# Performance work log

Hardware: AMD Instinct MI355X
Metric: run time of the kernel (lower is better)

Reference implementation:

```python
import jax, jax.numpy as jnp
import numpy as np

F, V, D, B = 3, 512, 8192, 64


def setup_inputs() -> dict:
    key = jax.random.key(0)
    k1, k2 = jax.random.split(key)
    # bipolar (MAP) codebooks: (f, v, d) in {-1, +1}
    codebooks = jnp.sign(jax.random.normal(k1, (F, V, D), dtype=jnp.float32))
    codebooks = jnp.where(codebooks == 0, 1.0, codebooks)
    # ground-truth factors -> inputs = bind (elementwise product) of one codevector per factor
    idx = jax.random.randint(k2, (B, F), 0, V)
    picked = codebooks[jnp.arange(F)[None, :], idx]          # (b, f, d)
    inputs = jnp.prod(picked, axis=1)                         # (b, d)
    # init estimates: bundle (superposition) of each codebook, signed, broadcast to batch
    init = jnp.sign(jnp.sum(codebooks, axis=1))               # (f, d)
    init = jnp.where(init == 0, 1.0, init)
    init_estimates = jnp.broadcast_to(init, (B, F, D)).astype(jnp.float32)
    return {"inputs": inputs, "init_estimates": init_estimates,
            "codebooks": codebooks, "iterations": 10}


def reference(inputs, init_estimates, codebooks, iterations):
    f = init_estimates.shape[-2]

    def step(est):
        # MAP inverse is identity; inv_others[:, j] = prod_{i != j} est[:, i]
        rolled = jnp.stack([jnp.roll(est, i, axis=-2) for i in range(1, f)], axis=-2)  # (b,f,f-1,d)
        inv_others = jnp.prod(rolled, axis=-2)                 # (b, f, d)  multibind
        new_est = inputs[:, None, :] * inv_others              # bind       (b, f, d)
        sim = jnp.einsum('bfd,fvd->bfv', new_est, codebooks)   # codebook similarity
        return jnp.sign(jnp.einsum('bfv,fvd->bfd', sim, codebooks))

    def cond(c):
        est, old, cnt, done = c
        return (cnt < iterations) & jnp.logical_not(done)

    def body(c):
        est, old, cnt, done = c
        new = step(est)
        done = jnp.all(new == old)
        return (new, new, cnt + 1, done)

    carry0 = (init_estimates, init_estimates, jnp.int32(0), jnp.array(False))
    est, _, cnt, _ = jax.lax.while_loop(cond, body, carry0)

    # cleanup: nearest codevector per factor (argmax dot similarity)
    sims = jnp.einsum('bfd,fvd->bfv', est, codebooks)
    outcome = jnp.argmax(sims, axis=-1)                        # (b, f) int indices
    return outcome, cnt - 1
```

## Files before the change

kernel.cpp:

```cpp
#include <hip/hip_runtime.h>

#define F 3
#define V 512
#define D 8192
#define B 64
#define ITERS 10
#define DW 256

typedef __bf16 bf16_t;
typedef __bf16 bf16x8 __attribute__((ext_vector_type(8)));
typedef float f32x4 __attribute__((ext_vector_type(4)));
typedef unsigned int u32;
typedef unsigned long long u64;


__global__ __launch_bounds__(256) void k_init_tr(const float* __restrict__ Csrc,
                                                 bf16_t* __restrict__ CbT,
                                                 u32* __restrict__ Cbits) {
  int f = blockIdx.z, vt = blockIdx.y, dt = blockIdx.x;
  __shared__ bf16_t tile[64 * 65];
  int t = threadIdx.x;
  int lane = t & 63;
  int v0 = vt * 64, d0 = dt * 64;
#pragma unroll
  for (int p = 0; p < 16; ++p) {
    int q = t + 256 * p;
    int i = q >> 6, j = q & 63;
    float x = Csrc[((long)(f * V + v0 + i)) * D + d0 + j];
    tile[i * 65 + j] = (bf16_t)x;
    u64 bal = __ballot(x < 0.f);
    if (lane == 0) {
      int v = v0 + i;
      uint2 wp;
      wp.x = (u32)(bal & 0xffffffffull);
      wp.y = (u32)(bal >> 32);
      *(uint2*)&Cbits[(((f * 64 + (dt >> 1)) * 512) + v) * 4 + (dt & 1) * 2] = wp;
    }
  }
  __syncthreads();
#pragma unroll
  for (int p = 0; p < 16; ++p) {
    int q = t + 256 * p;
    int jj = q >> 6, ii = q & 63;
    CbT[((long)f * D + d0 + jj) * V + v0 + ii] = tile[ii * 65 + jj];
  }
}

__global__ void k_init_pack(const float* __restrict__ inputs, const float* __restrict__ ie,
                            u32* __restrict__ in_bits, u32* __restrict__ es0,
                            u32* __restrict__ ez0, int* __restrict__ flags) {
  int tid = blockIdx.x * blockDim.x + threadIdx.x;
  int lane = tid & 63;
  int gw = tid >> 6;
  int NW = (gridDim.x * blockDim.x) >> 6;
  const int IN_W = B * (D / 64);
  const int EST_W = B * F * (D / 64);
  for (int c = gw; c < IN_W + EST_W; c += NW) {
    if (c < IN_W) {
      int b = c >> 7, dc = c & 127;
      float x = inputs[(long)b * D + dc * 64 + lane];
      u64 bal = __ballot(x < 0.f);
      if (lane == 0) {
        in_bits[b * DW + dc * 2] = (u32)(bal & 0xffffffffull);
        in_bits[b * DW + dc * 2 + 1] = (u32)(bal >> 32);
      }
    } else {
      int cc = c - IN_W;
      int bf = cc >> 7, dc = cc & 127;
      float x = ie[(long)bf * D + dc * 64 + lane];
      u64 bs = __ballot(x < 0.f);
      u64 bz = __ballot(x == 0.f);
      if (lane == 0) {
        es0[bf * DW + dc * 2] = (u32)(bs & 0xffffffffull);
        es0[bf * DW + dc * 2 + 1] = (u32)(bs >> 32);
        ez0[bf * DW + dc * 2] = (u32)(bz & 0xffffffffull);
        ez0[bf * DW + dc * 2 + 1] = (u32)(bz >> 32);
      }
    }
  }
  if (tid < 32) flags[tid] = 0;
}

__global__ __launch_bounds__(256) void k_sim(const u32* __restrict__ Cbits,
                                             const u32* __restrict__ in_bits,
                                             const u32* __restrict__ es0,
                                             const u32* __restrict__ ez0,
                                             const u32* __restrict__ es1,
                                             const u32* __restrict__ ez1,
                                             int* __restrict__ simBase,
                                             const int* __restrict__ anydiff,
                                             const int* __restrict__ hzp, int iter) {
  const int t = threadIdx.x, lane = t & 63;
  const int gw = blockIdx.x * 4 + (t >> 6);
  const int vg = gw & 7, bp = (gw >> 3) & 31, f = gw >> 8;
  const int b0 = bp * 2;
  const bool is_final = (iter >= ITERS);
  const u32 *es, *ez;
  int* sim;
  if (is_final) {
    int first0 = ITERS;
    for (int i = 0; i < ITERS; ++i)
      if (anydiff[i] == 0) { first0 = i; break; }
    int par = (first0 < ITERS) ? ((first0 + 1) & 1) : 0;
    es = par ? es1 : es0;
    ez = par ? ez1 : ez0;
    sim = simBase + ITERS * (F * B * V);
  } else {
    for (int i = 0; i < iter; ++i)
      if (anydiff[i] == 0) return;
    es = (iter & 1) ? es1 : es0;
    ez = (iter & 1) ? ez1 : ez0;
    sim = simBase + iter * (F * B * V);
  }
  const int hz = *hzp;

  u32 As0[4], As1[4], Az0[4], Az1[4];
  if (is_final) {
    const int i0 = (b0 * F + f) * DW, i1 = ((b0 + 1) * F + f) * DW;
#pragma unroll
    for (int r = 0; r < 4; ++r) {
      int o = r * 64 + lane;
      As0[r] = es[i0 + o];
      As1[r] = es[i1 + o];
    }
    if (hz) {
#pragma unroll
      for (int r = 0; r < 4; ++r) {
        int o = r * 64 + lane;
        Az0[r] = ~ez[i0 + o];
        Az1[r] = ~ez[i1 + o];
      }
    }
  } else {
    const int f1 = (f + 1) % 3, f2 = (f + 2) % 3;
    const int a0 = (b0 * F + f1) * DW, a1 = (b0 * F + f2) * DW;
    const int c0 = ((b0 + 1) * F + f1) * DW, c1 = ((b0 + 1) * F + f2) * DW;
    const int n0 = b0 * DW, n1 = (b0 + 1) * DW;
#pragma unroll
    for (int r = 0; r < 4; ++r) {
      int o = r * 64 + lane;
      As0[r] = in_bits[n0 + o] ^ es[a0 + o] ^ es[a1 + o];
      As1[r] = in_bits[n1 + o] ^ es[c0 + o] ^ es[c1 + o];
    }
    if (hz) {
#pragma unroll
      for (int r = 0; r < 4; ++r) {
        int o = r * 64 + lane;
        Az0[r] = ~(ez[a0 + o] | ez[a1 + o]);
        Az1[r] = ~(ez[c0 + o] | ez[c1 + o]);
      }
    }
  }

  int nzc0 = D, nzc1 = D;
  if (hz) {
    int p0 = 0, p1 = 0;
#pragma unroll
    for (int r = 0; r < 4; ++r) {
      p0 += __popc(Az0[r]);
      p1 += __popc(Az1[r]);
    }
    for (int off = 32; off; off >>= 1) {
      p0 += __shfl_xor(p0, off, 64);
      p1 += __shfl_xor(p1, off, 64);
    }
    nzc0 = p0;
    nzc1 = p1;
  }

  int acc0 = 0, acc1 = 0;
  const uint4* Cp = (const uint4*)Cbits + ((long)f * 64) * 512 + vg * 64 + lane;
  if (!hz) {
#pragma unroll
    for (int r = 0; r < 4; ++r) {
#pragma unroll
      for (int i = 0; i < 16; ++i) {
        uint4 c = Cp[(r * 16 + i) * 512];
        const int k = i * 4;
        u32 a;
        a = (u32)__builtin_amdgcn_readlane((int)As0[r], k + 0); acc0 += __popc(c.x ^ a);
        a = (u32)__builtin_amdgcn_readlane((int)As0[r], k + 1); acc0 += __popc(c.y ^ a);
        a = (u32)__builtin_amdgcn_readlane((int)As0[r], k + 2); acc0 += __popc(c.z ^ a);
        a = (u32)__builtin_amdgcn_readlane((int)As0[r], k + 3); acc0 += __popc(c.w ^ a);
        a = (u32)__builtin_amdgcn_readlane((int)As1[r], k + 0); acc1 += __popc(c.x ^ a);
        a = (u32)__builtin_amdgcn_readlane((int)As1[r], k + 1); acc1 += __popc(c.y ^ a);
        a = (u32)__builtin_amdgcn_readlane((int)As1[r], k + 2); acc1 += __popc(c.z ^ a);
        a = (u32)__builtin_amdgcn_readlane((int)As1[r], k + 3); acc1 += __popc(c.w ^ a);
      }
    }
  } else {
#pragma unroll
    for (int r = 0; r < 4; ++r) {
#pragma unroll
      for (int i = 0; i < 16; ++i) {
        uint4 c = Cp[(r * 16 + i) * 512];
        const int k = i * 4;
        u32 a, z;
        a = (u32)__builtin_amdgcn_readlane((int)As0[r], k + 0);
        z = (u32)__builtin_amdgcn_readlane((int)Az0[r], k + 0); acc0 += __popc((c.x ^ a) & z);
        a = (u32)__builtin_amdgcn_readlane((int)As0[r], k + 1);
        z = (u32)__builtin_amdgcn_readlane((int)Az0[r], k + 1); acc0 += __popc((c.y ^ a) & z);
        a = (u32)__builtin_amdgcn_readlane((int)As0[r], k + 2);
        z = (u32)__builtin_amdgcn_readlane((int)Az0[r], k + 2); acc0 += __popc((c.z ^ a) & z);
        a = (u32)__builtin_amdgcn_readlane((int)As0[r], k + 3);
        z = (u32)__builtin_amdgcn_readlane((int)Az0[r], k + 3); acc0 += __popc((c.w ^ a) & z);
        a = (u32)__builtin_amdgcn_readlane((int)As1[r], k + 0);
        z = (u32)__builtin_amdgcn_readlane((int)Az1[r], k + 0); acc1 += __popc((c.x ^ a) & z);
        a = (u32)__builtin_amdgcn_readlane((int)As1[r], k + 1);
        z = (u32)__builtin_amdgcn_readlane((int)Az1[r], k + 1); acc1 += __popc((c.y ^ a) & z);
        a = (u32)__builtin_amdgcn_readlane((int)As1[r], k + 2);
        z = (u32)__builtin_amdgcn_readlane((int)Az1[r], k + 2); acc1 += __popc((c.z ^ a) & z);
        a = (u32)__builtin_amdgcn_readlane((int)As1[r], k + 3);
        z = (u32)__builtin_amdgcn_readlane((int)Az1[r], k + 3); acc1 += __popc((c.w ^ a) & z);
      }
    }
  }
  const int v = vg * 64 + lane;
  sim[(f * B + b0) * V + v] = nzc0 - 2 * acc0;
  sim[(f * B + b0 + 1) * V + v] = nzc1 - 2 * acc1;
}

__global__ __launch_bounds__(256) void k_upd(const int* __restrict__ simBase,
                                             const bf16_t* __restrict__ CbT,
                                             u32* __restrict__ es0, u32* __restrict__ ez0,
                                             u32* __restrict__ es1, u32* __restrict__ ez1,
                                             int* __restrict__ anydiff,
                                             int* __restrict__ hzp, int iter) {
  const int f = blockIdx.y;
  const int d0 = blockIdx.x * 128;
  for (int i = 0; i < iter; ++i)
    if (anydiff[i] == 0) return;
  const u32* esIn = (iter & 1) ? es1 : es0;
  const u32* ezIn = (iter & 1) ? ez1 : ez0;
  u32* esOut = (iter & 1) ? es0 : es1;
  u32* ezOut = (iter & 1) ? ez0 : ez1;
  const int* sim = simBase + iter * (F * B * V) + f * (B * V);

  __shared__ __attribute__((aligned(16))) bf16_t lAh[64 * 88];
  __shared__ __attribute__((aligned(16))) bf16_t lAl[64 * 88];
  __shared__ __attribute__((aligned(16))) bf16_t lB[128 * 88];

  const int t = threadIdx.x;
  const int lane = t & 63, w = t >> 6;
  const int lm = lane & 15, quad = lane >> 4;

  f32x4 zero = {0.f, 0.f, 0.f, 0.f};
  f32x4 accH[4][2], accL[4][2];
#pragma unroll
  for (int mt = 0; mt < 4; ++mt)
#pragma unroll
    for (int nt = 0; nt < 2; ++nt) { accH[mt][nt] = zero; accL[mt][nt] = zero; }

  for (int c = 0; c < 8; ++c) {
    const int vb = c * 64;
    __syncthreads();
#pragma unroll
    for (int p = 0; p < 2; ++p) {
      int q = t + 256 * p;
      int b = q >> 3, vv = (q & 7) * 8;
      const int* sp = sim + b * V + vb + vv;
#pragma unroll
      for (int i = 0; i < 8; ++i) {
        int si = sp[i];
        lAh[b * 88 + vv + i] = (bf16_t)(float)(si >> 8);
        lAl[b * 88 + vv + i] = (bf16_t)(float)(si & 255);
      }
    }
#pragma unroll
    for (int p = 0; p < 4; ++p) {
      int q = t + 256 * p;
      int r = q >> 3, vv = (q & 7) * 8;
      *(bf16x8*)&lB[r * 88 + vv] =
          *(const bf16x8*)(CbT + ((long)f * D + d0 + r) * V + vb + vv);
    }
    __syncthreads();
#pragma unroll
    for (int ks2 = 0; ks2 < 2; ++ks2) {
      const int kb = ks2 * 32 + quad * 8;
      bf16x8 bf0 = *(const bf16x8*)&lB[(w * 32 + lm) * 88 + kb];
      bf16x8 bf1 = *(const bf16x8*)&lB[(w * 32 + 16 + lm) * 88 + kb];
#pragma unroll
      for (int mt = 0; mt < 4; ++mt) {
        bf16x8 ah = *(const bf16x8*)&lAh[(mt * 16 + lm) * 88 + kb];
        bf16x8 al = *(const bf16x8*)&lAl[(mt * 16 + lm) * 88 + kb];
        accH[mt][0] = __builtin_amdgcn_mfma_f32_16x16x32_bf16(ah, bf0, accH[mt][0], 0, 0, 0);
        accH[mt][1] = __builtin_amdgcn_mfma_f32_16x16x32_bf16(ah, bf1, accH[mt][1], 0, 0, 0);
        accL[mt][0] = __builtin_amdgcn_mfma_f32_16x16x32_bf16(al, bf0, accL[mt][0], 0, 0, 0);
        accL[mt][1] = __builtin_amdgcn_mfma_f32_16x16x32_bf16(al, bf1, accL[mt][1], 0, 0, 0);
      }
    }
  }
  const int W = blockIdx.x * 4 + w;
  bool anyd = false, zf = false;
#pragma unroll
  for (int mt = 0; mt < 4; ++mt)
#pragma unroll
    for (int r = 0; r < 4; ++r) {
      float v0 = 256.f * accH[mt][0][r] + accL[mt][0][r];
      float v1 = 256.f * accH[mt][1][r] + accL[mt][1][r];
      u64 s0 = __ballot(v0 < 0.f);
      u64 s1 = __ballot(v1 < 0.f);
      u64 z0 = __ballot(v0 == 0.f);
      u64 z1 = __ballot(v1 == 0.f);
      zf |= ((z0 | z1) != 0ull);
      if (lm == 0) {
        u32 ws = (u32)((s0 >> (quad * 16)) & 0xffffull) |
                 (((u32)((s1 >> (quad * 16)) & 0xffffull)) << 16);
        u32 wz = (u32)((z0 >> (quad * 16)) & 0xffffull) |
                 (((u32)((z1 >> (quad * 16)) & 0xffffull)) << 16);
        int b = mt * 16 + quad * 4 + r;
        int idx = (b * F + f) * DW + W;
        esOut[idx] = ws;
        ezOut[idx] = wz;
        anyd |= (esIn[idx] != ws) || (ezIn[idx] != wz);
      }
    }
  if (__any(anyd) && lane == 0) atomicOr(&anydiff[iter], 1);
  if (zf && lane == 0) atomicOr(hzp, 1);
}

__global__ __launch_bounds__(64) void k_out(const int* __restrict__ simBase,
                                            const int* __restrict__ anydiff,
                                            int* __restrict__ out) {
  const int* sim = simBase + ITERS * (F * B * V);
  int bid = blockIdx.x;
  int b = bid / F, f = bid % F;
  int lane = threadIdx.x;
  const int* row = sim + (f * B + b) * V;
  int best = -2147483647;
  int bidx = 0;
#pragma unroll
  for (int i = 0; i < V / 64; ++i) {
    int v = lane + 64 * i;
    int x = row[v];
    if (x > best) { best = x; bidx = v; }
  }
  for (int off = 32; off; off >>= 1) {
    int ov = __shfl_down(best, off, 64);
    int oi = __shfl_down(bidx, off, 64);
    if (ov > best || (ov == best && oi < bidx)) { best = ov; bidx = oi; }
  }
  if (lane == 0) out[b * F + f] = bidx;
  if (bid == 0 && lane == 0) {
    int first0 = ITERS;
    for (int i = 0; i < ITERS; ++i) {
      if (anydiff[i] == 0) { first0 = i; break; }
    }
    int cnt = (first0 < ITERS) ? (first0 + 1) : ITERS;
    out[B * F] = cnt - 1;
  }
}

extern "C" void kernel_launch(void* const* d_in, const int* in_sizes, int n_in,
                              void* d_out, int out_size, void* d_ws, size_t ws_size,
                              hipStream_t stream) {
  const float* inputs    = (const float*)d_in[0];
  const float* init_est  = (const float*)d_in[1];
  const float* codebooks = (const float*)d_in[2];

  char* w = (char*)d_ws;
  size_t o = 0;
  auto alloc = [&](size_t bytes) -> void* {
    void* p = w + o;
    o = (o + bytes + 255) & ~(size_t)255;
    return p;
  };
  bf16_t* CbT  = (bf16_t*)alloc((size_t)F * D * V * 2);
  u32* Cbits   = (u32*)alloc((size_t)F * 64 * 512 * 4 * 4);
  u32* in_bits = (u32*)alloc((size_t)B * DW * 4);
  u32* es0     = (u32*)alloc((size_t)B * F * DW * 4);
  u32* ez0     = (u32*)alloc((size_t)B * F * DW * 4);
  u32* es1     = (u32*)alloc((size_t)B * F * DW * 4);
  u32* ez1     = (u32*)alloc((size_t)B * F * DW * 4);
  int* simBase = (int*)alloc((size_t)(ITERS + 1) * F * B * V * 4);
  int* flags   = (int*)alloc(128);
  int* anydiff = flags;
  int* hz      = flags + 16;

  k_init_tr<<<dim3(128, 8, 3), 256, 0, stream>>>(codebooks, CbT, Cbits);
  k_init_pack<<<1024, 256, 0, stream>>>(inputs, init_est, in_bits, es0, ez0, flags);

  for (int j = 0; j < ITERS; ++j) {
    k_sim<<<192, 256, 0, stream>>>(Cbits, in_bits, es0, ez0, es1, ez1, simBase, anydiff, hz, j);
    k_upd<<<dim3(64, 3), 256, 0, stream>>>(simBase, CbT, es0, ez0, es1, ez1, anydiff, hz, j);
  }
  k_sim<<<192, 256, 0, stream>>>(Cbits, in_bits, es0, ez0, es1, ez1, simBase, anydiff, hz, ITERS);
  k_out<<<B * F, 64, 0, stream>>>(simBase, anydiff, (int*)d_out);
}
```

Before: 498.6 us.

## Bit-pack transposed codebook for update GEMM and double wave counts per block

The update kernel now reads the transposed codebook as packed sign bits (1 bit per entry instead of a bf16) and expands them in registers to ±1 bf16 values before the MFMA. This removes the bf16 transposed-codebook buffer, which was the main global-memory read each iteration. The similarity and update kernels now use 512 threads with one batch row per wave, and a single sim buffer is reused across iterations instead of one per iteration. The hz flag is now set during init packing, and the sim loads are vectorized. The cost is extra ALU work for unpacking bits and different occupancy per block.

New measurement: 533.9 us. 7.1% more time.

```diff
diff --git a/kernel.cpp b/kernel.cpp
--- a/kernel.cpp
+++ b/kernel.cpp
@@ -11,17 +11,21 @@
 typedef __bf16 bf16x8 __attribute__((ext_vector_type(8)));
 typedef float f32x4 __attribute__((ext_vector_type(4)));
 typedef unsigned int u32;
+typedef unsigned short u16;
+typedef u16 u16x8 __attribute__((ext_vector_type(8)));
 typedef unsigned long long u64;
 
 
 __global__ __launch_bounds__(256) void k_init_tr(const float* __restrict__ Csrc,
-                                                 bf16_t* __restrict__ CbT,
-                                                 u32* __restrict__ Cbits) {
+                                                 u32* __restrict__ Cbits,
+                                                 u32* __restrict__ CbTb,
+                                                 int* __restrict__ flags) {
   int f = blockIdx.z, vt = blockIdx.y, dt = blockIdx.x;
   __shared__ bf16_t tile[64 * 65];
   int t = threadIdx.x;
   int lane = t & 63;
   int v0 = vt * 64, d0 = dt * 64;
+  if (f == 0 && vt == 0 && dt == 0 && t < 32) flags[t] = 0;
 #pragma unroll
   for (int p = 0; p < 16; ++p) {
     int q = t + 256 * p;
@@ -42,7 +46,15 @@
   for (int p = 0; p < 16; ++p) {
     int q = t + 256 * p;
     int jj = q >> 6, ii = q & 63;
-    CbT[((long)f * D + d0 + jj) * V + v0 + ii] = tile[ii * 65 + jj];
+    float xv = (float)tile[ii * 65 + jj];
+    u64 bal = __ballot(xv < 0.f);
+    if (lane == 0) {
+      int d = d0 + jj;
+      uint2 wp;
+      wp.x = (u32)(bal & 0xffffffffull);
+      wp.y = (u32)(bal >> 32);
+      *(uint2*)&CbTb[((long)f * D + d) * 16 + vt * 2] = wp;
+    }
   }
 }
 
@@ -75,101 +87,78 @@
         es0[bf * DW + dc * 2 + 1] = (u32)(bs >> 32);
         ez0[bf * DW + dc * 2] = (u32)(bz & 0xffffffffull);
         ez0[bf * DW + dc * 2 + 1] = (u32)(bz >> 32);
-      }
-    }
-  }
-  if (tid < 32) flags[tid] = 0;
-}
-
-__global__ __launch_bounds__(256) void k_sim(const u32* __restrict__ Cbits,
+        if (bz) atomicOr(&flags[16], 1);
+      }
+    }
+  }
+}
+
+__global__ __launch_bounds__(512) void k_sim(const u32* __restrict__ Cbits,
                                              const u32* __restrict__ in_bits,
                                              const u32* __restrict__ es0,
                                              const u32* __restrict__ ez0,
                                              const u32* __restrict__ es1,
                                              const u32* __restrict__ ez1,
-                                             int* __restrict__ simBase,
-                                             const int* __restrict__ anydiff,
-                                             const int* __restrict__ hzp, int iter) {
-  const int t = threadIdx.x, lane = t & 63;
-  const int gw = blockIdx.x * 4 + (t >> 6);
-  const int vg = gw & 7, bp = (gw >> 3) & 31, f = gw >> 8;
-  const int b0 = bp * 2;
+                                             int* __restrict__ sim,
+                                             const int* __restrict__ flags, int iter) {
+  const int t = threadIdx.x, lane = t & 63, w = t >> 6;
+  const int gw = blockIdx.x * 8 + w;
+  const int vg = gw & 7, b = (gw >> 3) & 63, fs = gw >> 9;
   const bool is_final = (iter >= ITERS);
   const u32 *es, *ez;
-  int* sim;
   if (is_final) {
     int first0 = ITERS;
     for (int i = 0; i < ITERS; ++i)
-      if (anydiff[i] == 0) { first0 = i; break; }
+      if (flags[i] == 0) { first0 = i; break; }
     int par = (first0 < ITERS) ? ((first0 + 1) & 1) : 0;
     es = par ? es1 : es0;
     ez = par ? ez1 : ez0;
-    sim = simBase + ITERS * (F * B * V);
   } else {
     for (int i = 0; i < iter; ++i)
-      if (anydiff[i] == 0) return;
+      if (flags[i] == 0) return;
     es = (iter & 1) ? es1 : es0;
     ez = (iter & 1) ? ez1 : ez0;
-    sim = simBase + iter * (F * B * V);
-  }
-  const int hz = *hzp;
-
-  u32 As0[4], As1[4], Az0[4], Az1[4];
+  }
+  const int hz = flags[16];
+
+  u32 As[4], Az[4];
   if (is_final) {
-    const int i0 = (b0 * F + f) * DW, i1 = ((b0 + 1) * F + f) * DW;
+    const int i0 = (b * F + fs) * DW;
+#pragma unroll
+    for (int r = 0; r < 4; ++r) As[r] = es[i0 + r * 64 + lane];
+    if (hz) {
+#pragma unroll
+      for (int r = 0; r < 4; ++r) Az[r] = ~ez[i0 + r * 64 + lane];
+    }
+  } else {
+    const int f1 = (fs + 1) % 3, f2 = (fs + 2) % 3;
+    const int a0 = (b * F + f1) * DW, a1 = (b * F + f2) * DW;
+    const int n0 = b * DW;
 #pragma unroll
     for (int r = 0; r < 4; ++r) {
       int o = r * 64 + lane;
-      As0[r] = es[i0 + o];
-      As1[r] = es[i1 + o];
+      As[r] = in_bits[n0 + o] ^ es[a0 + o] ^ es[a1 + o];
     }
     if (hz) {
 #pragma unroll
       for (int r = 0; r < 4; ++r) {
         int o = r * 64 + lane;
-        Az0[r] = ~ez[i0 + o];
-        Az1[r] = ~ez[i1 + o];
-      }
-    }
-  } else {
-    const int f1 = (f + 1) % 3, f2 = (f + 2) % 3;
-    const int a0 = (b0 * F + f1) * DW, a1 = (b0 * F + f2) * DW;
-    const int c0 = ((b0 + 1) * F + f1) * DW, c1 = ((b0 + 1) * F + f2) * DW;
-    const int n0 = b0 * DW, n1 = (b0 + 1) * DW;
-#pragma unroll
-    for (int r = 0; r < 4; ++r) {
-      int o = r * 64 + lane;
-      As0[r] = in_bits[n0 + o] ^ es[a0 + o] ^ es[a1 + o];
-      As1[r] = in_bits[n1 + o] ^ es[c0 + o] ^ es[c1 + o];
-    }
-    if (hz) {
-#pragma unroll
-      for (int r = 0; r < 4; ++r) {
-        int o = r * 64 + lane;
-        Az0[r] = ~(ez[a0 + o] | ez[a1 + o]);
-        Az1[r] = ~(ez[c0 + o] | ez[c1 + o]);
-      }
-    }
-  }
-
-  int nzc0 = D, nzc1 = D;
+        Az[r] = ~(ez[a0 + o] | ez[a1 + o]);
+      }
+    }
+  }
+
+  int nzc = D;
   if (hz) {
-    int p0 = 0, p1 = 0;
-#pragma unroll
-    for (int r = 0; r < 4; ++r) {
-      p0 += __popc(Az0[r]);
-      p1 += __popc(Az1[r]);
-    }
-    for (int off = 32; off; off >>= 1) {
-      p0 += __shfl_xor(p0, off, 64);
-      p1 += __shfl_xor(p1, off, 64);
-    }
-    nzc0 = p0;
-    nzc1 = p1;
-  }
-
-  int acc0 = 0, acc1 = 0;
-  const uint4* Cp = (const uint4*)Cbits + ((long)f * 64) * 512 + vg * 64 + lane;
+    int p0 = 0;
+#pragma unroll
+    for (int r = 0; r < 4; ++r) p0 += __popc(Az[r]);
+    for (int off = 32; off; off >>= 1) p0 += __shfl_xor(p0, off, 64);
+    nzc = p0;
+  }
+
+  int acc = 0;
+  const uint4* Cp = (const uint4*)Cbits + ((long)fs * 64) * 512 + vg * 64 + lane;
   if (!hz) {
 #pragma unroll
     for (int r = 0; r < 4; ++r) {
@@ -178,14 +167,10 @@
         uint4 c = Cp[(r * 16 + i) * 512];
         const int k = i * 4;
         u32 a;
-        a = (u32)__builtin_amdgcn_readlane((int)As0[r], k + 0); acc0 += __popc(c.x ^ a);
-        a = (u32)__builtin_amdgcn_readlane((int)As0[r], k + 1); acc0 += __popc(c.y ^ a);
-        a = (u32)__builtin_amdgcn_readlane((int)As0[r], k + 2); acc0 += __popc(c.z ^ a);
-        a = (u32)__builtin_amdgcn_readlane((int)As0[r], k + 3); acc0 += __popc(c.w ^ a);
-        a = (u32)__builtin_amdgcn_readlane((int)As1[r], k + 0); acc1 += __popc(c.x ^ a);
-        a = (u32)__builtin_amdgcn_readlane((int)As1[r], k + 1); acc1 += __popc(c.y ^ a);
-        a = (u32)__builtin_amdgcn_readlane((int)As1[r], k + 2); acc1 += __popc(c.z ^ a);
-        a = (u32)__builtin_amdgcn_readlane((int)As1[r], k + 3); acc1 += __popc(c.w ^ a);
+        a = (u32)__builtin_amdgcn_readlane((int)As[r], k + 0); acc += __popc(c.x ^ a);
+        a = (u32)__builtin_amdgcn_readlane((int)As[r], k + 1); acc += __popc(c.y ^ a);
+        a = (u32)__builtin_amdgcn_readlane((int)As[r], k + 2); acc += __popc(c.z ^ a);
+        a = (u32)__builtin_amdgcn_readlane((int)As[r], k + 3); acc += __popc(c.w ^ a);
       }
     }
   } else {
@@ -196,45 +181,34 @@
         uint4 c = Cp[(r * 16 + i) * 512];
         const int k = i * 4;
         u32 a, z;
-        a = (u32)__builtin_amdgcn_readlane((int)As0[r], k + 0);
-        z = (u32)__builtin_amdgcn_readlane((int)Az0[r], k + 0); acc0 += __popc((c.x ^ a) & z);
-        a = (u32)__builtin_amdgcn_readlane((int)As0[r], k + 1);
-        z = (u32)__builtin_amdgcn_readlane((int)Az0[r], k + 1); acc0 += __popc((c.y ^ a) & z);
-        a = (u32)__builtin_amdgcn_readlane((int)As0[r], k + 2);
-        z = (u32)__builtin_amdgcn_readlane((int)Az0[r], k + 2); acc0 += __popc((c.z ^ a) & z);
-        a = (u32)__builtin_amdgcn_readlane((int)As0[r], k + 3);
-        z = (u32)__builtin_amdgcn_readlane((int)Az0[r], k + 3); acc0 += __popc((c.w ^ a) & z);
-        a = (u32)__builtin_amdgcn_readlane((int)As1[r], k + 0);
-        z = (u32)__builtin_amdgcn_readlane((int)Az1[r], k + 0); acc1 += __popc((c.x ^ a) & z);
-        a = (u32)__builtin_amdgcn_readlane((int)As1[r], k + 1);
-        z = (u32)__builtin_amdgcn_readlane((int)Az1[r], k + 1); acc1 += __popc((c.y ^ a) & z);
-        a = (u32)__builtin_amdgcn_readlane((int)As1[r], k + 2);
-        z = (u32)__builtin_amdgcn_readlane((int)Az1[r], k + 2); acc1 += __popc((c.z ^ a) & z);
-        a = (u32)__builtin_amdgcn_readlane((int)As1[r], k + 3);
-        z = (u32)__builtin_amdgcn_readlane((int)Az1[r], k + 3); acc1 += __popc((c.w ^ a) & z);
-      }
-    }
-  }
-  const int v = vg * 64 + lane;
-  sim[(f * B + b0) * V + v] = nzc0 - 2 * acc0;
-  sim[(f * B + b0 + 1) * V + v] = nzc1 - 2 * acc1;
-}
-
-__global__ __launch_bounds__(256) void k_upd(const int* __restrict__ simBase,
-                                             const bf16_t* __restrict__ CbT,
+        a = (u32)__builtin_amdgcn_readlane((int)As[r], k + 0);
+        z = (u32)__builtin_amdgcn_readlane((int)Az[r], k + 0); acc += __popc((c.x ^ a) & z);
+        a = (u32)__builtin_amdgcn_readlane((int)As[r], k + 1);
+        z = (u32)__builtin_amdgcn_readlane((int)Az[r], k + 1); acc += __popc((c.y ^ a) & z);
+        a = (u32)__builtin_amdgcn_readlane((int)As[r], k + 2);
+        z = (u32)__builtin_amdgcn_readlane((int)Az[r], k + 2); acc += __popc((c.z ^ a) & z);
+        a = (u32)__builtin_amdgcn_readlane((int)As[r], k + 3);
+        z = (u32)__builtin_amdgcn_readlane((int)Az[r], k + 3); acc += __popc((c.w ^ a) & z);
+      }
+    }
+  }
+  sim[(fs * B + b) * V + vg * 64 + lane] = nzc - 2 * acc;
+}
+
+__global__ __launch_bounds__(512) void k_upd(const int* __restrict__ sim,
+                                             const u32* __restrict__ CbTb,
                                              u32* __restrict__ es0, u32* __restrict__ ez0,
                                              u32* __restrict__ es1, u32* __restrict__ ez1,
-                                             int* __restrict__ anydiff,
-                                             int* __restrict__ hzp, int iter) {
-  const int f = blockIdx.y;
-  const int d0 = blockIdx.x * 128;
+                                             int* __restrict__ flags, int iter) {
+  const int fu = blockIdx.x >> 6;
+  const int dt = blockIdx.x & 63, d0 = dt * 128;
   for (int i = 0; i < iter; ++i)
-    if (anydiff[i] == 0) return;
+    if (flags[i] == 0) return;
   const u32* esIn = (iter & 1) ? es1 : es0;
   const u32* ezIn = (iter & 1) ? ez1 : ez0;
   u32* esOut = (iter & 1) ? es0 : es1;
   u32* ezOut = (iter & 1) ? ez0 : ez1;
-  const int* sim = simBase + iter * (F * B * V) + f * (B * V);
+  const int* simf = sim + fu * (B * V);
 
   __shared__ __attribute__((aligned(16))) bf16_t lAh[64 * 88];
   __shared__ __attribute__((aligned(16))) bf16_t lAl[64 * 88];
@@ -243,61 +217,68 @@
   const int t = threadIdx.x;
   const int lane = t & 63, w = t >> 6;
   const int lm = lane & 15, quad = lane >> 4;
+  const int wd = w & 3, wm = w >> 2;
 
   f32x4 zero = {0.f, 0.f, 0.f, 0.f};
-  f32x4 accH[4][2], accL[4][2];
-#pragma unroll
-  for (int mt = 0; mt < 4; ++mt)
-#pragma unroll
-    for (int nt = 0; nt < 2; ++nt) { accH[mt][nt] = zero; accL[mt][nt] = zero; }
+  f32x4 accH[2][2], accL[2][2];
+#pragma unroll
+  for (int m = 0; m < 2; ++m)
+#pragma unroll
+    for (int nt = 0; nt < 2; ++nt) { accH[m][nt] = zero; accL[m][nt] = zero; }
 
   for (int c = 0; c < 8; ++c) {
     const int vb = c * 64;
     __syncthreads();
+    {
+      int b8 = t >> 3, vv = (t & 7) * 8;
+      const int* sp = simf + b8 * V + vb + vv;
+      int4 sa = ((const int4*)sp)[0];
+      int4 sb = ((const int4*)sp)[1];
+      int si[8] = {sa.x, sa.y, sa.z, sa.w, sb.x, sb.y, sb.z, sb.w};
+#pragma unroll
+      for (int i = 0; i < 8; ++i) {
+        lAh[b8 * 88 + vv + i] = (bf16_t)(float)(si[i] >> 8);
+        lAl[b8 * 88 + vv + i] = (bf16_t)(float)(si[i] & 255);
+      }
+    }
 #pragma unroll
     for (int p = 0; p < 2; ++p) {
-      int q = t + 256 * p;
-      int b = q >> 3, vv = (q & 7) * 8;
-      const int* sp = sim + b * V + vb + vv;
-#pragma unroll
-      for (int i = 0; i < 8; ++i) {
-        int si = sp[i];
-        lAh[b * 88 + vv + i] = (bf16_t)(float)(si >> 8);
-        lAl[b * 88 + vv + i] = (bf16_t)(float)(si & 255);
-      }
-    }
-#pragma unroll
-    for (int p = 0; p < 4; ++p) {
-      int q = t + 256 * p;
+      int q = t + 512 * p;
       int r = q >> 3, vv = (q & 7) * 8;
-      *(bf16x8*)&lB[r * 88 + vv] =
-          *(const bf16x8*)(CbT + ((long)f * D + d0 + r) * V + vb + vv);
+      u32 bits = CbTb[((long)fu * D + d0 + r) * 16 + ((vb + vv) >> 5)];
+      int sh = (vb + vv) & 31;
+      u16x8 o;
+#pragma unroll
+      for (int i = 0; i < 8; ++i)
+        o[i] = (u16)(0x3F80u | (((bits >> (sh + i)) & 1u) << 15));
+      *(u16x8*)&lB[r * 88 + vv] = o;
     }
     __syncthreads();
 #pragma unroll
     for (int ks2 = 0; ks2 < 2; ++ks2) {
       const int kb = ks2 * 32 + quad * 8;
-      bf16x8 bf0 = *(const bf16x8*)&lB[(w * 32 + lm) * 88 + kb];
-      bf16x8 bf1 = *(const bf16x8*)&lB[(w * 32 + 16 + lm) * 88 + kb];
-#pragma unroll
-      for (int mt = 0; mt < 4; ++mt) {
+      bf16x8 bf0 = *(const bf16x8*)&lB[(wd * 32 + lm) * 88 + kb];
+      bf16x8 bf1 = *(const bf16x8*)&lB[(wd * 32 + 16 + lm) * 88 + kb];
+#pragma unroll
+      for (int m = 0; m < 2; ++m) {
+        const int mt = wm * 2 + m;
         bf16x8 ah = *(const bf16x8*)&lAh[(mt * 16 + lm) * 88 + kb];
         bf16x8 al = *(const bf16x8*)&lAl[(mt * 16 + lm) * 88 + kb];
-        accH[mt][0] = __builtin_amdgcn_mfma_f32_16x16x32_bf16(ah, bf0, accH[mt][0], 0, 0, 0);
-        accH[mt][1] = __builtin_amdgcn_mfma_f32_16x16x32_bf16(ah, bf1, accH[mt][1], 0, 0, 0);
-        accL[mt][0] = __builtin_amdgcn_mfma_f32_16x16x32_bf16(al, bf0, accL[mt][0], 0, 0, 0);
-        accL[mt][1] = __builtin_amdgcn_mfma_f32_16x16x32_bf16(al, bf1, accL[mt][1], 0, 0, 0);
-      }
-    }
-  }
-  const int W = blockIdx.x * 4 + w;
+        accH[m][0] = __builtin_amdgcn_mfma_f32_16x16x32_bf16(ah, bf0, accH[m][0], 0, 0, 0);
+        accH[m][1] = __builtin_amdgcn_mfma_f32_16x16x32_bf16(ah, bf1, accH[m][1], 0, 0, 0);
+        accL[m][0] = __builtin_amdgcn_mfma_f32_16x16x32_bf16(al, bf0, accL[m][0], 0, 0, 0);
+        accL[m][1] = __builtin_amdgcn_mfma_f32_16x16x32_bf16(al, bf1, accL[m][1], 0, 0, 0);
+      }
+    }
+  }
+  const int W = dt * 4 + wd;
   bool anyd = false, zf = false;
 #pragma unroll
-  for (int mt = 0; mt < 4; ++mt)
+  for (int m = 0; m < 2; ++m)
 #pragma unroll
     for (int r = 0; r < 4; ++r) {
-      float v0 = 256.f * accH[mt][0][r] + accL[mt][0][r];
-      float v1 = 256.f * accH[mt][1][r] + accL[mt][1][r];
+      float v0 = 256.f * accH[m][0][r] + accL[m][0][r];
+      float v1 = 256.f * accH[m][1][r] + accL[m][1][r];
       u64 s0 = __ballot(v0 < 0.f);
       u64 s1 = __ballot(v1 < 0.f);
       u64 z0 = __ballot(v0 == 0.f);
@@ -308,21 +289,20 @@
                  (((u32)((s1 >> (quad * 16)) & 0xffffull)) << 16);
         u32 wz = (u32)((z0 >> (quad * 16)) & 0xffffull) |
                  (((u32)((z1 >> (quad * 16)) & 0xffffull)) << 16);
-        int b = mt * 16 + quad * 4 + r;
-        int idx = (b * F + f) * DW + W;
+        int b = (wm * 2 + m) * 16 + quad * 4 + r;
+        int idx = (b * F + fu) * DW + W;
+        anyd |= (esIn[idx] != ws) || (ezIn[idx] != wz);
         esOut[idx] = ws;
         ezOut[idx] = wz;
-        anyd |= (esIn[idx] != ws) || (ezIn[idx] != wz);
-      }
-    }
-  if (__any(anyd) && lane == 0) atomicOr(&anydiff[iter], 1);
-  if (zf && lane == 0) atomicOr(hzp, 1);
-}
-
-__global__ __launch_bounds__(64) void k_out(const int* __restrict__ simBase,
-                                            const int* __restrict__ anydiff,
+      }
+    }
+  if (__any(anyd) && lane == 0) atomicOr(&flags[iter], 1);
+  if (zf && lane == 0) atomicOr(&flags[16], 1);
+}
+
+__global__ __launch_bounds__(64) void k_out(const int* __restrict__ sim,
+                                            const int* __restrict__ flags,
                                             int* __restrict__ out) {
-  const int* sim = simBase + ITERS * (F * B * V);
   int bid = blockIdx.x;
   int b = bid / F, f = bid % F;
   int lane = threadIdx.x;
@@ -344,7 +324,7 @@
   if (bid == 0 && lane == 0) {
     int first0 = ITERS;
     for (int i = 0; i < ITERS; ++i) {
-      if (anydiff[i] == 0) { first0 = i; break; }
+      if (flags[i] == 0) { first0 = i; break; }
     }
     int cnt = (first0 < ITERS) ? (first0 + 1) : ITERS;
     out[B * F] = cnt - 1;
@@ -365,25 +345,23 @@
     o = (o + bytes + 255) & ~(size_t)255;
     return p;
   };
-  bf16_t* CbT  = (bf16_t*)alloc((size_t)F * D * V * 2);
   u32* Cbits   = (u32*)alloc((size_t)F * 64 * 512 * 4 * 4);
+  u32* CbTb    = (u32*)alloc((size_t)F * D * 16 * 4);
   u32* in_bits = (u32*)alloc((size_t)B * DW * 4);
   u32* es0     = (u32*)alloc((size_t)B * F * DW * 4);
   u32* ez0     = (u32*)alloc((size_t)B * F * DW * 4);
   u32* es1     = (u32*)alloc((size_t)B * F * DW * 4);
   u32* ez1     = (u32*)alloc((size_t)B * F * DW * 4);
-  int* simBase = (int*)alloc((size_t)(ITERS + 1) * F * B * V * 4);
+  int* sim     = (int*)alloc((size_t)F * B * V * 4);
   int* flags   = (int*)alloc(128);
-  int* anydiff = flags;
-  int* hz      = flags + 16;
-
-  k_init_tr<<<dim3(128, 8, 3), 256, 0, stream>>>(codebooks, CbT, Cbits);
+
+  k_init_tr<<<dim3(128, 8, 3), 256, 0, stream>>>(codebooks, Cbits, CbTb, flags);
   k_init_pack<<<1024, 256, 0, stream>>>(inputs, init_est, in_bits, es0, ez0, flags);
 
   for (int j = 0; j < ITERS; ++j) {
-    k_sim<<<192, 256, 0, stream>>>(Cbits, in_bits, es0, ez0, es1, ez1, simBase, anydiff, hz, j);
-    k_upd<<<dim3(64, 3), 256, 0, stream>>>(simBase, CbT, es0, ez0, es1, ez1, anydiff, hz, j);
-  }
-  k_sim<<<192, 256, 0, stream>>>(Cbits, in_bits, es0, ez0, es1, ez1, simBase, anydiff, hz, ITERS);
-  k_out<<<B * F, 64, 0, stream>>>(simBase, anydiff, (int*)d_out);
-}
+    k_sim<<<192, 512, 0, stream>>>(Cbits, in_bits, es0, ez0, es1, ez1, sim, flags, j);
+    k_upd<<<192, 512, 0, stream>>>(sim, CbTb, es0, ez0, es1, ez1, flags, j);
+  }
+  k_sim<<<192, 512, 0, stream>>>(Cbits, in_bits, es0, ez0, es1, ez1, sim, flags, ITERS);
+  k_out<<<B * F, 64, 0, stream>>>(sim, flags, (int*)d_out);
+}
```
